# Performance work log

Measured on AMD Instinct MI355X. Metric: run time of the kernel, lower is better.

The kernel has to match this reference:

```python
import jax, jax.numpy as jnp
import numpy as np

NUM_POINTS = 100000
BATCH = 4096
K = 10


def setup_inputs() -> dict:
    key = jax.random.key(0)
    k1, k2, k3, k4, k5 = jax.random.split(key, 5)
    rays_o = jax.random.normal(k1, (BATCH, 3), dtype=jnp.float32)
    rays_d = jax.random.normal(k2, (BATCH, 3), dtype=jnp.float32)
    xyz = jax.random.normal(k3, (NUM_POINTS, 3), dtype=jnp.float32) * 0.1
    features_dc = jax.random.normal(k4, (NUM_POINTS, 1, 3), dtype=jnp.float32)
    opacity = jax.random.normal(k5, (NUM_POINTS, 1), dtype=jnp.float32)
    return {"rays_o": rays_o, "rays_d": rays_d, "xyz": xyz,
            "features_dc": features_dc, "opacity": opacity}


def reference(rays_o, rays_d, xyz, features_dc, opacity):
    # colors = sigmoid(features[:,0,:]) ; features[:,0,:] == features_dc[:,0,:]
    colors = jax.nn.sigmoid(features_dc[:, 0, :])          # [N,3]
    op = jax.nn.sigmoid(opacity[:, 0])                      # [N]
    ray_centers = rays_o + rays_d * 3.0                     # [B,3]
    # Euclidean cdist via ||a||^2 + ||b||^2 - 2 a.b (matmul form, like torch.cdist p=2)
    sq = (jnp.sum(ray_centers * ray_centers, axis=1)[:, None]
          + jnp.sum(xyz * xyz, axis=1)[None, :]
          - 2.0 * ray_centers @ xyz.T)                      # [B,N]
    distances = jnp.sqrt(jnp.maximum(sq, 0.0))
    # top-K smallest distances per ray
    _, idx = jax.lax.top_k(-distances, K)                   # [B,K]
    d_sel = jnp.take_along_axis(distances, idx, axis=1)     # [B,K]
    w = jnp.exp(-d_sel * 0.1) * op[idx]                     # [B,K]
    w = w / (jnp.sum(w, axis=1, keepdims=True) + 1e-8)
    rgb = jnp.einsum('bk,bkc->bc', w, colors[idx])          # [B,3]
    return rgb
```

## Files before the change

kernel.cpp:

```cpp
#include <hip/hip_runtime.h>
#include <math.h>

#define NPTS   100000
#define NRAYS  4096
#define KTOP   10
#define KMER   12
#define CAP    128
#define LCAP   12

#define PPAIR  4
#define SBLK   49
#define RCS    64
#define RPBS   (NRAYS / RCS)

#define TPAIR  4
#define NPART  64
#define TRAYS  8
#define TGRP   16

typedef float v2f __attribute__((ext_vector_type(2)));

static_assert(SBLK * 2048 >= NPTS, "scan covers all points");
static_assert(TGRP * 2048 <= NPTS, "theta sample within real points");

__device__ __forceinline__ float4 make_center(const float* __restrict__ ro,
                                              const float* __restrict__ rd,
                                              int ray, float w) {
    float ox = ro[3 * ray + 0], oy = ro[3 * ray + 1], oz = ro[3 * ray + 2];
    float dx = rd[3 * ray + 0], dy = rd[3 * ray + 1], dz = rd[3 * ray + 2];
    float cx, cy, cz;
    {
#pragma clang fp contract(off)
        cx = ox + dx * 3.0f;
        cy = oy + dy * 3.0f;
        cz = oz + dz * 3.0f;
    }
    return make_float4(cx, cy, cz, w);
}

__device__ __forceinline__ float sigm(float x) { return 1.0f / (1.0f + expf(-x)); }

__device__ __forceinline__ unsigned long long mkkey(float sc, int id, bool v) {
    unsigned u = __float_as_uint(sc);
    u = (u & 0x80000000u) ? ~u : (u | 0x80000000u);
    unsigned long long k = ((unsigned long long)u << 32) | (unsigned)(~id);
    return v ? k : 0ull;
}

__global__ __launch_bounds__(256, 2) void theta_kernel(const float* __restrict__ xyz,
                                                       const float* __restrict__ ro,
                                                       const float* __restrict__ rd,
                                                       float* __restrict__ theta,
                                                       int* __restrict__ cnt) {
    __shared__ float4 rsh[TRAYS];
    __shared__ float  Msh[4][TRAYS][64];
    const int tid = threadIdx.x, wave = tid >> 6, lane = tid & 63;
    const int rbase = blockIdx.x * TRAYS;

    if (tid < TRAYS) rsh[tid] = make_center(ro, rd, rbase + tid, 0.0f);
    __syncthreads();

    float4 rr[TRAYS];
#pragma unroll
    for (int r = 0; r < TRAYS; ++r) rr[r] = rsh[r];

    v2f M[TRAYS];
#pragma unroll
    for (int r = 0; r < TRAYS; ++r) M[r] = (v2f){-INFINITY, -INFINITY};

#pragma unroll 1
    for (int g = 0; g < TGRP; ++g) {
        const int id0 = g * 2048 + wave * 512 + lane;
        v2f px[TPAIR], py[TPAIR], pz[TPAIR], pw[TPAIR];
#pragma unroll
        for (int u = 0; u < TPAIR; ++u) {
            int ia = id0 + (2 * u) * 64, ib = id0 + (2 * u + 1) * 64;
            float xa = xyz[3 * ia + 0], ya = xyz[3 * ia + 1], za = xyz[3 * ia + 2];
            float xb = xyz[3 * ib + 0], yb = xyz[3 * ib + 1], zb = xyz[3 * ib + 2];
            px[u] = (v2f){xa, xb}; py[u] = (v2f){ya, yb}; pz[u] = (v2f){za, zb};
            pw[u] = (v2f){-0.5f * fmaf(xa, xa, fmaf(ya, ya, za * za)),
                          -0.5f * fmaf(xb, xb, fmaf(yb, yb, zb * zb))};
        }
#pragma unroll
        for (int r = 0; r < TRAYS; ++r) {
            const v2f rx = (v2f){rr[r].x, rr[r].x};
            const v2f ry = (v2f){rr[r].y, rr[r].y};
            const v2f rz = (v2f){rr[r].z, rr[r].z};
            v2f m = M[r];
#pragma unroll
            for (int u = 0; u < TPAIR; ++u) {
                v2f t = __builtin_elementwise_fma(pz[u], rz, pw[u]);
                t = __builtin_elementwise_fma(py[u], ry, t);
                t = __builtin_elementwise_fma(px[u], rx, t);
                m = __builtin_elementwise_max(m, t);
            }
            M[r] = m;
        }
    }

#pragma unroll
    for (int r = 0; r < TRAYS; ++r)
        Msh[wave][r][lane] = fmaxf(M[r].x, M[r].y);
    __syncthreads();

    if (tid < TRAYS) {
        float vs[KTOP];
#pragma unroll
        for (int j = 0; j < KTOP; ++j) vs[j] = -INFINITY;
#pragma unroll 1
        for (int p = 0; p < NPART; ++p) {
            float v = fmaxf(fmaxf(Msh[0][tid][p], Msh[1][tid][p]),
                            fmaxf(Msh[2][tid][p], Msh[3][tid][p]));
#pragma unroll
            for (int t = KTOP - 1; t >= 1; --t) {
                bool up = v > vs[t - 1], here = v > vs[t];
                vs[t] = up ? vs[t - 1] : (here ? v : vs[t]);
            }
            vs[0] = fmaxf(vs[0], v);
        }
        theta[rbase + tid] = vs[KTOP - 1];
        cnt[rbase + tid] = 0;
    }
}

__global__ __launch_bounds__(256) void scan_kernel(const float* __restrict__ xyz,
                                                   const float* __restrict__ ro,
                                                   const float* __restrict__ rd,
                                                   const float* __restrict__ theta,
                                                   int* __restrict__ cnt,
                                                   float2* __restrict__ cand) {
    __shared__ float4 rsh[RPBS];
    __shared__ int    lcnt[RPBS];
    __shared__ float2 lbuf[RPBS][LCAP];
    const int pblk = blockIdx.x, rchunk = blockIdx.y;
    const int tid = threadIdx.x, wave = tid >> 6, lane = tid & 63;
    const int rbase = rchunk * RPBS;

    if (tid < RPBS) {
        rsh[tid] = make_center(ro, rd, rbase + tid, theta[rbase + tid]);
        lcnt[tid] = 0;
    }

    const int id0 = pblk * 2048 + wave * 512 + lane;
    v2f px[PPAIR], py[PPAIR], pz[PPAIR], pw[PPAIR];
#pragma unroll
    for (int u = 0; u < PPAIR; ++u) {
        int ia = id0 + (2 * u) * 64, ib = id0 + (2 * u + 1) * 64;
        bool va = ia < NPTS, vb = ib < NPTS;
        int ca = va ? ia : 0, cb = vb ? ib : 0;
        float xa = xyz[3 * ca + 0], ya = xyz[3 * ca + 1], za = xyz[3 * ca + 2];
        float xb = xyz[3 * cb + 0], yb = xyz[3 * cb + 1], zb = xyz[3 * cb + 2];
        px[u] = (v2f){xa, xb}; py[u] = (v2f){ya, yb}; pz[u] = (v2f){za, zb};
        pw[u] = (v2f){va ? -0.5f * fmaf(xa, xa, fmaf(ya, ya, za * za)) : -INFINITY,
                      vb ? -0.5f * fmaf(xb, xb, fmaf(yb, yb, zb * zb)) : -INFINITY};
    }
    __syncthreads();

    auto emit = [&](int r, float sc, int id) {
        int slot = atomicAdd(&lcnt[r], 1);
        float2 e = make_float2(sc, __int_as_float(id));
        if (slot < LCAP) lbuf[r][slot] = e;
        else {
            int gs = atomicAdd(&cnt[rbase + r], 1);
            if (gs < CAP) cand[((rbase + r) << 7) + gs] = e;
        }
    };

#pragma unroll 4
    for (int r = 0; r < RPBS; ++r) {
        float4 rp = rsh[r];
        const v2f rx = (v2f){rp.x, rp.x}, ry = (v2f){rp.y, rp.y}, rz = (v2f){rp.z, rp.z};
        v2f s[PPAIR];
        v2f a0, a1;
        {
            v2f t = __builtin_elementwise_fma(pz[0], rz, pw[0]);
            t = __builtin_elementwise_fma(py[0], ry, t);
            t = __builtin_elementwise_fma(px[0], rx, t);
            s[0] = t; a0 = t;
            t = __builtin_elementwise_fma(pz[1], rz, pw[1]);
            t = __builtin_elementwise_fma(py[1], ry, t);
            t = __builtin_elementwise_fma(px[1], rx, t);
            s[1] = t; a1 = t;
            t = __builtin_elementwise_fma(pz[2], rz, pw[2]);
            t = __builtin_elementwise_fma(py[2], ry, t);
            t = __builtin_elementwise_fma(px[2], rx, t);
            s[2] = t; a0 = __builtin_elementwise_max(a0, t);
            t = __builtin_elementwise_fma(pz[3], rz, pw[3]);
            t = __builtin_elementwise_fma(py[3], ry, t);
            t = __builtin_elementwise_fma(px[3], rx, t);
            s[3] = t; a1 = __builtin_elementwise_max(a1, t);
        }
        v2f am = __builtin_elementwise_max(a0, a1);
        float hm = fmaxf(am.x, am.y);

        if (__ballot(hm >= rp.w)) {
#pragma unroll
            for (int u = 0; u < PPAIR; ++u) {
                if (__ballot(s[u].x >= rp.w)) {
                    if (s[u].x >= rp.w) emit(r, s[u].x, id0 + (2 * u) * 64);
                }
                if (__ballot(s[u].y >= rp.w)) {
                    if (s[u].y >= rp.w) emit(r, s[u].y, id0 + (2 * u + 1) * 64);
                }
            }
        }
    }

    __syncthreads();
    if (tid < RPBS) {
        int n = lcnt[tid];
        n = n < LCAP ? n : LCAP;
        if (n > 0) {
            const int rayid = rbase + tid;
            int base = atomicAdd(&cnt[rayid], n);
            for (int j = 0; j < n; ++j) {
                int slot = base + j;
                if (slot < CAP) cand[(rayid << 7) + slot] = lbuf[tid][j];
            }
        }
    }
}

__global__ __launch_bounds__(256) void merge_kernel(const float* __restrict__ ro,
                                                    const float* __restrict__ rd,
                                                    const int* __restrict__ cnt,
                                                    const float2* __restrict__ cand,
                                                    const float* __restrict__ xyz,
                                                    const float* __restrict__ fdc,
                                                    const float* __restrict__ opac,
                                                    float* __restrict__ out) {
    const int wave = threadIdx.x >> 6, lane = threadIdx.x & 63;
    const int ray = blockIdx.x * 4 + wave;

    int n = cnt[ray];
    n = n < CAP ? n : CAP;

    const float2* cl = cand + (ray << 7);
    float2 e0 = cl[lane];
    float2 e1 = cl[64 + lane];
    int id0 = __float_as_int(e0.y), id1 = __float_as_int(e1.y);

    unsigned long long k0 = mkkey(e0.x, id0, lane < n);
    unsigned long long k1 = mkkey(e1.x, id1, lane + 64 < n);

    int sel = -1;
    unsigned long long kl = k0 > k1 ? k0 : k1;
#pragma unroll
    for (int j = 0; j < KMER; ++j) {
        unsigned long long m = kl;
#pragma unroll
        for (int off = 1; off < 64; off <<= 1) {
            unsigned long long o = __shfl_xor(m, off);
            m = m > o ? m : o;
        }
        bool win = (kl == m) && (m != 0ull);
        int wid = (k0 >= k1) ? id0 : id1;
        unsigned long long wmask = __ballot(win);
        int wl = __ffsll(wmask) - 1;
        int bid = __shfl(wid, wl & 63);
        if (m == 0ull) bid = -1;
        if (lane == j) sel = bid;
        if (win) {
            if (k0 >= k1) k0 = 0ull; else k1 = 0ull;
            kl = k0 > k1 ? k0 : k1;
        }
    }

    float ox = ro[3 * ray + 0], oy = ro[3 * ray + 1], oz = ro[3 * ray + 2];
    float dx = rd[3 * ray + 0], dy = rd[3 * ray + 1], dz = rd[3 * ray + 2];
    float cxf, cyf, czf;
    {
#pragma clang fp contract(off)
        cxf = ox + dx * 3.0f;
        cyf = oy + dy * 3.0f;
        czf = oz + dz * 3.0f;
    }
    double Cx = (double)cxf, Cy = (double)cyf, Cz = (double)czf;
    double cn = Cx * Cx + Cy * Cy + Cz * Cz;

    bool valid = (lane < KMER) && (sel >= 0);
    int pid = valid ? sel : 0;
    double X = (double)xyz[3 * pid + 0];
    double Y = (double)xyz[3 * pid + 1];
    double Z = (double)xyz[3 * pid + 2];
    double sq = valid ? (cn + (X * X + Y * Y + Z * Z) - 2.0 * (Cx * X + Cy * Y + Cz * Z))
                      : (double)INFINITY;
    int cid = valid ? sel : 0x7fffffff;

    int rank = 0;
#pragma unroll
    for (int k = 0; k < KMER; ++k) {
        double sk = __shfl(sq, k);
        int    ik = __shfl(cid, k);
        if ((sk < sq) || (sk == sq && ik < cid)) ++rank;
    }

    bool take = valid && (rank < KTOP);
    float w = 0.0f, rr = 0.0f, gg = 0.0f, bb = 0.0f;
    if (take) {
        float dd = sqrtf(fmaxf((float)sq, 0.0f));
        w  = expf(-0.1f * dd) * sigm(opac[pid]);
        rr = w * sigm(fdc[3 * pid + 0]);
        gg = w * sigm(fdc[3 * pid + 1]);
        bb = w * sigm(fdc[3 * pid + 2]);
    }
#pragma unroll
    for (int off = 1; off < 64; off <<= 1) {
        w  += __shfl_xor(w,  off);
        rr += __shfl_xor(rr, off);
        gg += __shfl_xor(gg, off);
        bb += __shfl_xor(bb, off);
    }
    if (lane == 0) {
        float inv = 1.0f / (w + 1e-8f);
        out[3 * ray + 0] = rr * inv;
        out[3 * ray + 1] = gg * inv;
        out[3 * ray + 2] = bb * inv;
    }
}

extern "C" void kernel_launch(void* const* d_in, const int* in_sizes, int n_in,
                              void* d_out, int out_size, void* d_ws, size_t ws_size,
                              hipStream_t stream) {
    const float* rays_o = (const float*)d_in[0];
    const float* rays_d = (const float*)d_in[1];
    const float* xyz    = (const float*)d_in[2];
    const float* fdc    = (const float*)d_in[3];
    const float* opac   = (const float*)d_in[4];
    float* out = (float*)d_out;

    char* w = (char*)d_ws;
    float*  theta  = (float*)w;  w += (size_t)NRAYS * 4;
    int*    cnt    = (int*)w;    w += (size_t)NRAYS * 4;
    float2* cand   = (float2*)w;

    theta_kernel<<<NRAYS / TRAYS, 256, 0, stream>>>(xyz, rays_o, rays_d, theta, cnt);
    scan_kernel<<<dim3(SBLK, RCS), 256, 0, stream>>>(xyz, rays_o, rays_d, theta, cnt, cand);
    merge_kernel<<<NRAYS / 4, 256, 0, stream>>>(rays_o, rays_d, cnt, cand, xyz, fdc, opac, out);
}
```

Measured before the change: 151.5 us.

## Double points per scan thread and unroll theta kernel point groups

```diff
diff --git a/kernel.cpp b/kernel.cpp
--- a/kernel.cpp
+++ b/kernel.cpp
@@ -8,8 +8,8 @@
 #define CAP    128
 #define LCAP   12
 
-#define PPAIR  4
-#define SBLK   49
+#define PPAIR  8
+#define SBLK   25
 #define RCS    64
 #define RPBS   (NRAYS / RCS)
 
@@ -20,7 +20,7 @@
 
 typedef float v2f __attribute__((ext_vector_type(2)));
 
-static_assert(SBLK * 2048 >= NPTS, "scan covers all points");
+static_assert(SBLK * 4096 >= NPTS, "scan covers all points");
 static_assert(TGRP * 2048 <= NPTS, "theta sample within real points");
 
 __device__ __forceinline__ float4 make_center(const float* __restrict__ ro,
@@ -69,17 +69,20 @@
     for (int r = 0; r < TRAYS; ++r) M[r] = (v2f){-INFINITY, -INFINITY};
 
 #pragma unroll 1
-    for (int g = 0; g < TGRP; ++g) {
-        const int id0 = g * 2048 + wave * 512 + lane;
-        v2f px[TPAIR], py[TPAIR], pz[TPAIR], pw[TPAIR];
-#pragma unroll
-        for (int u = 0; u < TPAIR; ++u) {
-            int ia = id0 + (2 * u) * 64, ib = id0 + (2 * u + 1) * 64;
-            float xa = xyz[3 * ia + 0], ya = xyz[3 * ia + 1], za = xyz[3 * ia + 2];
-            float xb = xyz[3 * ib + 0], yb = xyz[3 * ib + 1], zb = xyz[3 * ib + 2];
-            px[u] = (v2f){xa, xb}; py[u] = (v2f){ya, yb}; pz[u] = (v2f){za, zb};
-            pw[u] = (v2f){-0.5f * fmaf(xa, xa, fmaf(ya, ya, za * za)),
-                          -0.5f * fmaf(xb, xb, fmaf(yb, yb, zb * zb))};
+    for (int g = 0; g < TGRP; g += 2) {
+        v2f px[2][TPAIR], py[2][TPAIR], pz[2][TPAIR], pw[2][TPAIR];
+#pragma unroll
+        for (int h = 0; h < 2; ++h) {
+            const int id0 = (g + h) * 2048 + wave * 512 + lane;
+#pragma unroll
+            for (int u = 0; u < TPAIR; ++u) {
+                int ia = id0 + (2 * u) * 64, ib = id0 + (2 * u + 1) * 64;
+                float xa = xyz[3 * ia + 0], ya = xyz[3 * ia + 1], za = xyz[3 * ia + 2];
+                float xb = xyz[3 * ib + 0], yb = xyz[3 * ib + 1], zb = xyz[3 * ib + 2];
+                px[h][u] = (v2f){xa, xb}; py[h][u] = (v2f){ya, yb}; pz[h][u] = (v2f){za, zb};
+                pw[h][u] = (v2f){-0.5f * fmaf(xa, xa, fmaf(ya, ya, za * za)),
+                                 -0.5f * fmaf(xb, xb, fmaf(yb, yb, zb * zb))};
+            }
         }
 #pragma unroll
         for (int r = 0; r < TRAYS; ++r) {
@@ -88,11 +91,14 @@
             const v2f rz = (v2f){rr[r].z, rr[r].z};
             v2f m = M[r];
 #pragma unroll
-            for (int u = 0; u < TPAIR; ++u) {
-                v2f t = __builtin_elementwise_fma(pz[u], rz, pw[u]);
-                t = __builtin_elementwise_fma(py[u], ry, t);
-                t = __builtin_elementwise_fma(px[u], rx, t);
-                m = __builtin_elementwise_max(m, t);
+            for (int h = 0; h < 2; ++h) {
+#pragma unroll
+                for (int u = 0; u < TPAIR; ++u) {
+                    v2f t = __builtin_elementwise_fma(pz[h][u], rz, pw[h][u]);
+                    t = __builtin_elementwise_fma(py[h][u], ry, t);
+                    t = __builtin_elementwise_fma(px[h][u], rx, t);
+                    m = __builtin_elementwise_max(m, t);
+                }
             }
             M[r] = m;
         }
@@ -123,12 +129,12 @@
     }
 }
 
-__global__ __launch_bounds__(256) void scan_kernel(const float* __restrict__ xyz,
-                                                   const float* __restrict__ ro,
-                                                   const float* __restrict__ rd,
-                                                   const float* __restrict__ theta,
-                                                   int* __restrict__ cnt,
-                                                   float2* __restrict__ cand) {
+__global__ __launch_bounds__(256, 2) void scan_kernel(const float* __restrict__ xyz,
+                                                      const float* __restrict__ ro,
+                                                      const float* __restrict__ rd,
+                                                      const float* __restrict__ theta,
+                                                      int* __restrict__ cnt,
+                                                      float2* __restrict__ cand) {
     __shared__ float4 rsh[RPBS];
     __shared__ int    lcnt[RPBS];
     __shared__ float2 lbuf[RPBS][LCAP];
@@ -141,7 +147,7 @@
         lcnt[tid] = 0;
     }
 
-    const int id0 = pblk * 2048 + wave * 512 + lane;
+    const int id0 = pblk * 4096 + wave * 1024 + lane;
     v2f px[PPAIR], py[PPAIR], pz[PPAIR], pw[PPAIR];
 #pragma unroll
     for (int u = 0; u < PPAIR; ++u) {
@@ -166,29 +172,22 @@
         }
     };
 
-#pragma unroll 4
+#pragma unroll 2
     for (int r = 0; r < RPBS; ++r) {
         float4 rp = rsh[r];
         const v2f rx = (v2f){rp.x, rp.x}, ry = (v2f){rp.y, rp.y}, rz = (v2f){rp.z, rp.z};
         v2f s[PPAIR];
         v2f a0, a1;
-        {
-            v2f t = __builtin_elementwise_fma(pz[0], rz, pw[0]);
-            t = __builtin_elementwise_fma(py[0], ry, t);
-            t = __builtin_elementwise_fma(px[0], rx, t);
-            s[0] = t; a0 = t;
-            t = __builtin_elementwise_fma(pz[1], rz, pw[1]);
-            t = __builtin_elementwise_fma(py[1], ry, t);
-            t = __builtin_elementwise_fma(px[1], rx, t);
-            s[1] = t; a1 = t;
-            t = __builtin_elementwise_fma(pz[2], rz, pw[2]);
-            t = __builtin_elementwise_fma(py[2], ry, t);
-            t = __builtin_elementwise_fma(px[2], rx, t);
-            s[2] = t; a0 = __builtin_elementwise_max(a0, t);
-            t = __builtin_elementwise_fma(pz[3], rz, pw[3]);
-            t = __builtin_elementwise_fma(py[3], ry, t);
-            t = __builtin_elementwise_fma(px[3], rx, t);
-            s[3] = t; a1 = __builtin_elementwise_max(a1, t);
+#pragma unroll
+        for (int u = 0; u < PPAIR; ++u) {
+            v2f t = __builtin_elementwise_fma(pz[u], rz, pw[u]);
+            t = __builtin_elementwise_fma(py[u], ry, t);
+            t = __builtin_elementwise_fma(px[u], rx, t);
+            s[u] = t;
+            if (u == 0)      a0 = t;
+            else if (u == 1) a1 = t;
+            else if (u & 1)  a1 = __builtin_elementwise_max(a1, t);
+            else             a0 = __builtin_elementwise_max(a0, t);
         }
         v2f am = __builtin_elementwise_max(a0, a1);
         float hm = fmaxf(am.x, am.y);
```

After: 170.9 us. +12.8%, slower.
